# Kernel optimization log

Hardware: AMD Instinct MI355X
Metric: run time of the kernel (lower is better)

## Reference

```python
import jax, jax.numpy as jnp
import numpy as np

EMBED = 1024
HEADS = 16
HEAD_DIM = EMBED // HEADS


def setup_inputs() -> dict:
    key = jax.random.key(0)
    ks = jax.random.split(key, 5)
    s = 1.0 / np.sqrt(EMBED)
    x = jax.random.normal(ks[0], (2, 2048, EMBED), dtype=jnp.float32)
    W_qkv = jax.random.uniform(ks[1], (EMBED, 3 * EMBED), dtype=jnp.float32, minval=-s, maxval=s)
    b_qkv = jax.random.uniform(ks[2], (3 * EMBED,), dtype=jnp.float32, minval=-s, maxval=s)
    W_out = jax.random.uniform(ks[3], (EMBED, EMBED), dtype=jnp.float32, minval=-s, maxval=s)
    b_out = jax.random.uniform(ks[4], (EMBED,), dtype=jnp.float32, minval=-s, maxval=s)
    return {"x": x, "W_qkv": W_qkv, "b_qkv": b_qkv, "W_out": W_out, "b_out": b_out}


def reference(x, W_qkv, b_qkv, W_out, b_out):
    B, S, E = x.shape
    qkv = x @ W_qkv + b_qkv                              # [B,S,3E]
    qkv = qkv.reshape(B, S, 3, HEADS, HEAD_DIM)
    q, k, v = qkv[:, :, 0], qkv[:, :, 1], qkv[:, :, 2]   # [B,S,H,D]
    q = q.transpose(0, 2, 1, 3)                          # [B,H,S,D]
    k = k.transpose(0, 2, 1, 3)
    v = v.transpose(0, 2, 1, 3)
    scale = 1.0 / np.sqrt(HEAD_DIM).astype(np.float32)
    scores = jnp.einsum('bhqd,bhkd->bhqk', q, k) * scale  # [B,H,S,S]
    causal = jnp.tril(jnp.ones((S, S), dtype=bool))
    scores = jnp.where(causal, scores, jnp.float32(-jnp.inf))
    attn = jax.nn.softmax(scores, axis=-1)
    out = jnp.einsum('bhqk,bhkd->bhqd', attn, v)          # [B,H,S,D]
    out = out.transpose(0, 2, 1, 3).reshape(B, S, E)
    return out @ W_out + b_out
```

## Files before the change

kernel.cpp:

```cpp
#include <hip/hip_runtime.h>
#include <hip/hip_bf16.h>
#include <math.h>

typedef __bf16 bf16;
typedef bf16 bf16x4 __attribute__((ext_vector_type(4)));
typedef bf16 bf16x8 __attribute__((ext_vector_type(8)));
typedef float f32x4 __attribute__((ext_vector_type(4)));
typedef float f32x16 __attribute__((ext_vector_type(16)));
typedef unsigned int uint;

#define EMB 1024
#define SEQ 2048
#define BATCH 2
#define NH 16
#define HD 64

#define SCALE2 0.18033688011112042f

__device__ __forceinline__ void glds16(const void* g, void* l) {
  __builtin_amdgcn_global_load_lds(
      (__attribute__((address_space(1))) void*)g,
      (__attribute__((address_space(3))) void*)l, 16, 0, 0);
}

__device__ __forceinline__ uint cvtpk(float lo, float hi) {
  uint r;
  asm("v_cvt_pk_bf16_f32 %0, %1, %2" : "=v"(r) : "v"(lo), "v"(hi));
  return r;
}
__device__ __forceinline__ void plswap(uint& a, uint& b) {
  asm("v_permlane32_swap_b32 %0, %1" : "+v"(a), "+v"(b));
}

__global__ __launch_bounds__(256) void cvt_f32_bf16(const float* __restrict__ in,
                                                    bf16* __restrict__ out, int n) {
  int i = (blockIdx.x * 256 + threadIdx.x) * 4;
  if (i < n) {
    float4 v = *reinterpret_cast<const float4*>(in + i);
    out[i + 0] = (bf16)v.x;
    out[i + 1] = (bf16)v.y;
    out[i + 2] = (bf16)v.z;
    out[i + 3] = (bf16)v.w;
  }
}

__global__ __launch_bounds__(256) void transpose_cvt(const float* __restrict__ in,
                                                     bf16* __restrict__ out,
                                                     int R, int C) {
  __shared__ float tile[32][33];
  int c0 = blockIdx.x * 32, r0 = blockIdx.y * 32;
  int tx = threadIdx.x, ty = threadIdx.y;
#pragma unroll
  for (int i = 0; i < 32; i += 8)
    tile[ty + i][tx] = in[(size_t)(r0 + ty + i) * C + c0 + tx];
  __syncthreads();
#pragma unroll
  for (int i = 0; i < 32; i += 8)
    out[(size_t)(c0 + ty + i) * R + r0 + tx] = (bf16)tile[tx][ty + i];
}

#define QBM 256
#define QBN 128
#define QBK 32

__global__ __launch_bounds__(512) void gemm_qkv(
    const bf16* __restrict__ A, const bf16* __restrict__ Bt,
    const float* __restrict__ bias, int M, int N, int K,
    bf16* __restrict__ outQ, bf16* __restrict__ outK, bf16* __restrict__ outVt) {
  __shared__ bf16 Alds[2][QBM * QBK];
  __shared__ bf16 Blds[2][QBN * QBK];

  const int t = threadIdx.x;
  const int lane = t & 63;
  const int w = t >> 6;
  const int wr = w >> 1, wc = w & 1;
  const int lg = lane >> 4, lr = lane & 15;
  const int m0 = blockIdx.y * QBM;
  const int n0 = blockIdx.x * QBN;

  const int ca0 = t, ca1 = t + 512;
  const int ra0 = ca0 >> 2, cha0 = ca0 & 3;
  const int ra1 = ca1 >> 2, cha1 = ca1 & 3;
  const int rb = t >> 2, chb = t & 3;

  const bf16* Arow0 = A + (size_t)(m0 + ra0) * K + cha0 * 8;
  const bf16* Arow1 = A + (size_t)(m0 + ra1) * K + cha1 * 8;
  const bf16* Brow  = Bt + (size_t)(n0 + rb) * K + chb * 8;

  f32x4 acc[4][4] = {};

  glds16(Arow0, &Alds[0][ca0 * 8]);
  glds16(Arow1, &Alds[0][ca1 * 8]);
  glds16(Brow, &Blds[0][t * 8]);

  int cur = 0;
  for (int k0 = 0; k0 < K; k0 += QBK) {
    if (k0 + QBK < K) {
      const int kn = k0 + QBK;
      const int nb = cur ^ 1;
      glds16(Arow0 + kn, &Alds[nb][ca0 * 8]);
      glds16(Arow1 + kn, &Alds[nb][ca1 * 8]);
      glds16(Brow + kn, &Blds[nb][t * 8]);
      asm volatile("s_waitcnt vmcnt(3)" ::: "memory");
    } else {
      asm volatile("s_waitcnt vmcnt(0)" ::: "memory");
    }
    __builtin_amdgcn_s_barrier();

    bf16x8 af[4], bfr[4];
#pragma unroll
    for (int i = 0; i < 4; ++i)
      af[i] = *reinterpret_cast<const bf16x8*>(
          &Alds[cur][(wr * 64 + i * 16 + lr) * QBK + lg * 8]);
#pragma unroll
    for (int j = 0; j < 4; ++j)
      bfr[j] = *reinterpret_cast<const bf16x8*>(
          &Blds[cur][(wc * 64 + j * 16 + lr) * QBK + lg * 8]);
#pragma unroll
    for (int i = 0; i < 4; ++i)
#pragma unroll
      for (int j = 0; j < 4; ++j)
        acc[i][j] = __builtin_amdgcn_mfma_f32_16x16x32_bf16(af[i], bfr[j], acc[i][j], 0, 0, 0);

    asm volatile("s_waitcnt lgkmcnt(0)" ::: "memory");
    __builtin_amdgcn_s_barrier();
    cur ^= 1;
  }

#pragma unroll
  for (int j = 0; j < 4; ++j) {
    const int n = n0 + wc * 64 + j * 16 + lr;
    const float bi = bias[n];
    const int which = n >> 10, rem = n & 1023;
    const int hh = rem >> 6, d = rem & 63;
#pragma unroll
    for (int i = 0; i < 4; ++i) {
      const int mb = m0 + wr * 64 + i * 16 + lg * 4;
      const int bb = mb >> 11, ss = mb & 2047;
      if (which == 2) {
        bf16x4 pv;
#pragma unroll
        for (int r = 0; r < 4; ++r) pv[r] = (bf16)(acc[i][j][r] + bi);
        *reinterpret_cast<bf16x4*>(
            outVt + (((size_t)bb * NH + hh) * HD + d) * SEQ + ss) = pv;
      } else if (which == 0) {
        bf16* dst = outQ + (((size_t)bb * NH + hh) * SEQ + ss) * HD + d;
#pragma unroll
        for (int r = 0; r < 4; ++r)
          dst[(size_t)r * HD] = (bf16)((acc[i][j][r] + bi) * SCALE2);
      } else {
        bf16* dst = outK + (((size_t)bb * NH + hh) * SEQ + ss) * HD + d;
#pragma unroll
        for (int r = 0; r < 4; ++r) dst[(size_t)r * HD] = (bf16)(acc[i][j][r] + bi);
      }
    }
  }
}

#define BM 128
#define BN 128
#define BK 32

__global__ __launch_bounds__(256) void gemm_proj(
    const bf16* __restrict__ A, const bf16* __restrict__ Bt,
    const float* __restrict__ bias, int M, int N, int K,
    float* __restrict__ outF) {
  __shared__ bf16 Alds[2][BM * BK];
  __shared__ bf16 Blds[2][BM * BK];

  const int t = threadIdx.x;
  const int lane = t & 63;
  const int w = t >> 6;
  const int wr = w >> 1, wc = w & 1;
  const int lg = lane >> 4, lr = lane & 15;
  const int m0 = blockIdx.y * BM;
  const int n0 = blockIdx.x * BN;

  const int c0 = w * 64 + lane;
  const int c1 = 256 + w * 64 + lane;
  const int r0 = c0 >> 2, ch0 = c0 & 3;
  const int r1 = c1 >> 2, ch1 = c1 & 3;

  const bf16* Arow0 = A + (size_t)(m0 + r0) * K + ch0 * 8;
  const bf16* Arow1 = A + (size_t)(m0 + r1) * K + ch1 * 8;
  const bf16* Brow0 = Bt + (size_t)(n0 + r0) * K + ch0 * 8;
  const bf16* Brow1 = Bt + (size_t)(n0 + r1) * K + ch1 * 8;

  f32x4 acc[4][4] = {};

  glds16(Arow0, &Alds[0][c0 * 8]);
  glds16(Arow1, &Alds[0][c1 * 8]);
  glds16(Brow0, &Blds[0][c0 * 8]);
  glds16(Brow1, &Blds[0][c1 * 8]);

  int cur = 0;
  for (int k0 = 0; k0 < K; k0 += BK) {
    if (k0 + BK < K) {
      const int kn = k0 + BK;
      const int nb = cur ^ 1;
      glds16(Arow0 + kn, &Alds[nb][c0 * 8]);
      glds16(Arow1 + kn, &Alds[nb][c1 * 8]);
      glds16(Brow0 + kn, &Blds[nb][c0 * 8]);
      glds16(Brow1 + kn, &Blds[nb][c1 * 8]);
      asm volatile("s_waitcnt vmcnt(4)" ::: "memory");
    } else {
      asm volatile("s_waitcnt vmcnt(0)" ::: "memory");
    }
    __builtin_amdgcn_s_barrier();

    bf16x8 af[4], bfr[4];
#pragma unroll
    for (int i = 0; i < 4; ++i)
      af[i] = *reinterpret_cast<const bf16x8*>(
          &Alds[cur][(wr * 64 + i * 16 + lr) * BK + lg * 8]);
#pragma unroll
    for (int j = 0; j < 4; ++j)
      bfr[j] = *reinterpret_cast<const bf16x8*>(
          &Blds[cur][(wc * 64 + j * 16 + lr) * BK + lg * 8]);
#pragma unroll
    for (int i = 0; i < 4; ++i)
#pragma unroll
      for (int j = 0; j < 4; ++j)
        acc[i][j] = __builtin_amdgcn_mfma_f32_16x16x32_bf16(af[i], bfr[j], acc[i][j], 0, 0, 0);

    asm volatile("s_waitcnt lgkmcnt(0)" ::: "memory");
    __builtin_amdgcn_s_barrier();
    cur ^= 1;
  }

#pragma unroll
  for (int j = 0; j < 4; ++j) {
    const int n = n0 + wc * 64 + j * 16 + lr;
    const float bi = bias[n];
#pragma unroll
    for (int i = 0; i < 4; ++i) {
      const int mb = m0 + wr * 64 + i * 16 + lg * 4;
#pragma unroll
      for (int r = 0; r < 4; ++r)
        outF[(size_t)(mb + r) * N + n] = acc[i][j][r] + bi;
    }
  }
}


#define STAGE(kt_, buf_)                                                       \
  {                                                                            \
    const int kb_ = (kt_) << 7;                                                \
    _Pragma("unroll")                                                          \
    for (int j = 0; j < 4; ++j) {                                              \
      const int g = j * 256 + t;                                               \
      const int rowK = g >> 3, ccK = g & 7;                                    \
      const int pcK = ((ccK ^ (rowK & 7)) << 3);                               \
      glds16(Kb + headoff + (size_t)(kb_ + rowK) * HD + pcK, &Kl[buf_][g * 8]);\
      const int rowV = g >> 4, ccV = g & 15;                                   \
      const int pcV = ((ccV ^ (rowV & 15)) << 3);                              \
      glds16(Vt + headoff + (size_t)rowV * SEQ + kb_ + pcV, &Vl[buf_][g * 8]); \
    }                                                                          \
  }

#define QK_ACC(SX, X)                                                          \
  if (!diag || (X) <= w) {                                                     \
    _Pragma("unroll")                                                          \
    for (int dd = 0; dd < 4; ++dd) {                                           \
      const int pcK = (((dd * 2 + hi) ^ swzK) << 3);                           \
      bf16x8 kf = *reinterpret_cast<const bf16x8*>(                            \
          &Kl[cur][((X) * 32 + l31) * 64 + pcK]);                              \
      SX = __builtin_amdgcn_mfma_f32_32x32x16_bf16(kf, qf[dd], SX, 0, 0, 0);   \
    }                                                                          \
  }

__global__ __launch_bounds__(256, 2) void attn_fwd(
    const bf16* __restrict__ Qb, const bf16* __restrict__ Kb,
    const bf16* __restrict__ Vt, bf16* __restrict__ Ob) {
  __shared__ bf16 Kl[2][128 * 64];
  __shared__ bf16 Vl[2][64 * 128];

  const int t = threadIdx.x;
  const int lane = t & 63;
  const int w = t >> 6;
  const int l31 = lane & 31;
  const int hi = lane >> 5;
  const int hi8 = hi << 3;
  const int swzK = l31 & 7;
  const int swzV = l31 & 15;

  const int id = blockIdx.x;
  const int qb = (id < 256) ? (15 - (id >> 5)) : ((id - 256) >> 5);
  const int bh = id & 31;
  const int h = bh & 15, b = bh >> 4;
  const size_t headoff = ((size_t)b * NH + h) * SEQ * HD;
  const int qrow = qb * 128 + w * 32 + l31;

  bf16x8 qf[4];
  {
    const bf16* qr = Qb + headoff + (size_t)qrow * HD + hi8;
#pragma unroll
    for (int d = 0; d < 4; ++d) qf[d] = *reinterpret_cast<const bf16x8*>(qr + d * 16);
  }

  bf16x8 ones;
#pragma unroll
  for (int i = 0; i < 8; ++i) ones[i] = (bf16)1.0f;

  f32x16 accO0 = {}, accO1 = {};
  f32x16 accL = {};
  const int nkt = qb + 1;

  STAGE(0, 0);

  for (int kt = 0; kt < nkt; ++kt) {
    const int cur = kt & 1;
    if (kt + 1 < nkt) {
      STAGE(kt + 1, cur ^ 1);
      asm volatile("s_waitcnt vmcnt(8)" ::: "memory");
    } else {
      asm volatile("s_waitcnt vmcnt(0)" ::: "memory");
    }
    __builtin_amdgcn_s_barrier();

    const bool diag = (kt == nkt - 1);
    f32x16 s0 = {}, s1 = {}, s2 = {}, s3 = {};
    __builtin_amdgcn_s_setprio(1);
    QK_ACC(s0, 0)
    QK_ACC(s1, 1)
    QK_ACC(s2, 2)
    QK_ACC(s3, 3)
    __builtin_amdgcn_s_setprio(0);
    if (diag) {
      const int kq = (kt << 7) + hi * 4 - qrow;
#pragma unroll
      for (int r = 0; r < 16; ++r) {
        const int off = (r & 3) + 8 * (r >> 2);
        if (kq + off > 0) s0[r] = -1e30f;
        if (kq + off + 32 > 0) s1[r] = -1e30f;
        if (kq + off + 64 > 0) s2[r] = -1e30f;
        if (kq + off + 96 > 0) s3[r] = -1e30f;
      }
    }
#pragma unroll
    for (int r = 0; r < 16; ++r) {
      s0[r] = __builtin_amdgcn_exp2f(s0[r]);
      s1[r] = __builtin_amdgcn_exp2f(s1[r]);
      s2[r] = __builtin_amdgcn_exp2f(s2[r]);
      s3[r] = __builtin_amdgcn_exp2f(s3[r]);
    }
    uint wv[32];
    wv[0]  = cvtpk(s0[0],  s0[1]);  wv[1]  = cvtpk(s0[2],  s0[3]);
    wv[2]  = cvtpk(s0[4],  s0[5]);  wv[3]  = cvtpk(s0[6],  s0[7]);
    wv[4]  = cvtpk(s0[8],  s0[9]);  wv[5]  = cvtpk(s0[10], s0[11]);
    wv[6]  = cvtpk(s0[12], s0[13]); wv[7]  = cvtpk(s0[14], s0[15]);
    wv[8]  = cvtpk(s1[0],  s1[1]);  wv[9]  = cvtpk(s1[2],  s1[3]);
    wv[10] = cvtpk(s1[4],  s1[5]);  wv[11] = cvtpk(s1[6],  s1[7]);
    wv[12] = cvtpk(s1[8],  s1[9]);  wv[13] = cvtpk(s1[10], s1[11]);
    wv[14] = cvtpk(s1[12], s1[13]); wv[15] = cvtpk(s1[14], s1[15]);
    wv[16] = cvtpk(s2[0],  s2[1]);  wv[17] = cvtpk(s2[2],  s2[3]);
    wv[18] = cvtpk(s2[4],  s2[5]);  wv[19] = cvtpk(s2[6],  s2[7]);
    wv[20] = cvtpk(s2[8],  s2[9]);  wv[21] = cvtpk(s2[10], s2[11]);
    wv[22] = cvtpk(s2[12], s2[13]); wv[23] = cvtpk(s2[14], s2[15]);
    wv[24] = cvtpk(s3[0],  s3[1]);  wv[25] = cvtpk(s3[2],  s3[3]);
    wv[26] = cvtpk(s3[4],  s3[5]);  wv[27] = cvtpk(s3[6],  s3[7]);
    wv[28] = cvtpk(s3[8],  s3[9]);  wv[29] = cvtpk(s3[10], s3[11]);
    wv[30] = cvtpk(s3[12], s3[13]); wv[31] = cvtpk(s3[14], s3[15]);
    plswap(wv[0], wv[2]);   plswap(wv[1], wv[3]);
    plswap(wv[4], wv[6]);   plswap(wv[5], wv[7]);
    plswap(wv[8], wv[10]);  plswap(wv[9], wv[11]);
    plswap(wv[12], wv[14]); plswap(wv[13], wv[15]);
    plswap(wv[16], wv[18]); plswap(wv[17], wv[19]);
    plswap(wv[20], wv[22]); plswap(wv[21], wv[23]);
    plswap(wv[24], wv[26]); plswap(wv[25], wv[27]);
    plswap(wv[28], wv[30]); plswap(wv[29], wv[31]);
    __builtin_amdgcn_s_setprio(1);
#pragma unroll
    for (int ks = 0; ks < 8; ++ks) {
      if (!diag || ks < 2 * w + 2) {
        uint4 u = make_uint4(wv[(ks >> 1) * 8 + (ks & 1) * 4],
                             wv[(ks >> 1) * 8 + (ks & 1) * 4 + 1],
                             wv[(ks >> 1) * 8 + (ks & 1) * 4 + 2],
                             wv[(ks >> 1) * 8 + (ks & 1) * 4 + 3]);
        bf16x8 pf = *reinterpret_cast<bf16x8*>(&u);
        const int pcV = (((ks * 2 + hi) ^ swzV) << 3);
        bf16x8 vf0 = *reinterpret_cast<const bf16x8*>(&Vl[cur][l31 * 128 + pcV]);
        bf16x8 vf1 = *reinterpret_cast<const bf16x8*>(&Vl[cur][(l31 + 32) * 128 + pcV]);
        accO0 = __builtin_amdgcn_mfma_f32_32x32x16_bf16(vf0, pf, accO0, 0, 0, 0);
        accO1 = __builtin_amdgcn_mfma_f32_32x32x16_bf16(vf1, pf, accO1, 0, 0, 0);
        accL  = __builtin_amdgcn_mfma_f32_32x32x16_bf16(ones, pf, accL, 0, 0, 0);
      }
    }
    __builtin_amdgcn_s_setprio(0);
    asm volatile("s_waitcnt lgkmcnt(0)" ::: "memory");
    __builtin_amdgcn_s_barrier();
  }

  const float inv = 1.0f / accL[0];
  bf16* orow = Ob + ((size_t)b * SEQ + qrow) * EMB + h * HD + hi * 4;
#pragma unroll
  for (int rq = 0; rq < 4; ++rq) {
    bf16x4 o0, o1;
#pragma unroll
    for (int i = 0; i < 4; ++i) {
      o0[i] = (bf16)(accO0[rq * 4 + i] * inv);
      o1[i] = (bf16)(accO1[rq * 4 + i] * inv);
    }
    *reinterpret_cast<bf16x4*>(orow + rq * 8) = o0;
    *reinterpret_cast<bf16x4*>(orow + 32 + rq * 8) = o1;
  }
}

extern "C" void kernel_launch(void* const* d_in, const int* in_sizes, int n_in,
                              void* d_out, int out_size, void* d_ws, size_t ws_size,
                              hipStream_t stream) {
  const float* x    = (const float*)d_in[0];
  const float* Wqkv = (const float*)d_in[1];
  const float* bqkv = (const float*)d_in[2];
  const float* Wout = (const float*)d_in[3];
  const float* bout = (const float*)d_in[4];
  float* out = (float*)d_out;

  char* ws = (char*)d_ws;
  bf16* xb     = (bf16*)(ws);
  bf16* wqkvt  = (bf16*)(ws + 8388608);
  bf16* woutt  = (bf16*)(ws + 14680064);
  bf16* Qb     = (bf16*)(ws + 16777216);
  bf16* Kb     = (bf16*)(ws + 25165824);
  bf16* Vtb    = (bf16*)(ws + 33554432);
  bf16* attnb  = (bf16*)(ws + 41943040);

  const int n1 = 4096 * 1024;
  cvt_f32_bf16<<<(n1 / 4 + 255) / 256, 256, 0, stream>>>(x, xb, n1);
  dim3 tb(32, 8);
  transpose_cvt<<<dim3(3072 / 32, 1024 / 32), tb, 0, stream>>>(Wqkv, wqkvt, 1024, 3072);
  transpose_cvt<<<dim3(1024 / 32, 1024 / 32), tb, 0, stream>>>(Wout, woutt, 1024, 1024);

  dim3 g1(3072 / QBN, 4096 / QBM);
  gemm_qkv<<<g1, 512, 0, stream>>>(xb, wqkvt, bqkv, 4096, 3072, 1024,
                                   Qb, Kb, Vtb);

  attn_fwd<<<512, 256, 0, stream>>>(Qb, Kb, Vtb, attnb);

  dim3 g2(1024 / BN, 4096 / BM);
  gemm_proj<<<g2, 256, 0, stream>>>(attnb, woutt, bout, 4096, 1024, 1024, out);
}
```

Measured before the change: 116.4 us.

## Split causal attention KV range across two blocks and add combine kernel

The attention kernel now splits each query block's key range into two halves handled by separate workgroups, doubling the grid. It shrinks the key tile from 128 to 64 and raises the occupancy hint to four blocks per CU. Each half writes unnormalized bf16 partial outputs and per-row sums. A new elementwise kernel adds the two partials and divides by the summed denominators. This aims to improve load balance and CU utilisation for the causal triangle. In exchange it adds an extra launch, extra global traffic for the partials, and a bf16 rounding of unnormalized values.

```diff
diff --git a/kernel.cpp b/kernel.cpp
--- a/kernel.cpp
+++ b/kernel.cpp
@@ -242,38 +242,27 @@
   }
 }
 
-
-#define STAGE(kt_, buf_)                                                       \
+#define AKT 64
+
+#define ASTAGE(kt_, buf_)                                                      \
   {                                                                            \
-    const int kb_ = (kt_) << 7;                                                \
+    const int kb_ = (kt_) << 6;                                                \
     _Pragma("unroll")                                                          \
-    for (int j = 0; j < 4; ++j) {                                              \
+    for (int j = 0; j < 2; ++j) {                                              \
       const int g = j * 256 + t;                                               \
-      const int rowK = g >> 3, ccK = g & 7;                                    \
-      const int pcK = ((ccK ^ (rowK & 7)) << 3);                               \
-      glds16(Kb + headoff + (size_t)(kb_ + rowK) * HD + pcK, &Kl[buf_][g * 8]);\
-      const int rowV = g >> 4, ccV = g & 15;                                   \
-      const int pcV = ((ccV ^ (rowV & 15)) << 3);                              \
-      glds16(Vt + headoff + (size_t)rowV * SEQ + kb_ + pcV, &Vl[buf_][g * 8]); \
+      const int row = g >> 3, cc = g & 7;                                      \
+      const int pc = ((cc ^ (row & 7)) << 3);                                  \
+      glds16(Kb + headoff + (size_t)(kb_ + row) * HD + pc, &Kl[buf_][g * 8]);  \
+      glds16(Vt + headoff + (size_t)row * SEQ + kb_ + pc, &Vl[buf_][g * 8]);   \
     }                                                                          \
   }
 
-#define QK_ACC(SX, X)                                                          \
-  if (!diag || (X) <= w) {                                                     \
-    _Pragma("unroll")                                                          \
-    for (int dd = 0; dd < 4; ++dd) {                                           \
-      const int pcK = (((dd * 2 + hi) ^ swzK) << 3);                           \
-      bf16x8 kf = *reinterpret_cast<const bf16x8*>(                            \
-          &Kl[cur][((X) * 32 + l31) * 64 + pcK]);                              \
-      SX = __builtin_amdgcn_mfma_f32_32x32x16_bf16(kf, qf[dd], SX, 0, 0, 0);   \
-    }                                                                          \
-  }
-
-__global__ __launch_bounds__(256, 2) void attn_fwd(
+__global__ __launch_bounds__(256, 4) void attn_fwd(
     const bf16* __restrict__ Qb, const bf16* __restrict__ Kb,
-    const bf16* __restrict__ Vt, bf16* __restrict__ Ob) {
-  __shared__ bf16 Kl[2][128 * 64];
-  __shared__ bf16 Vl[2][64 * 128];
+    const bf16* __restrict__ Vt, bf16* __restrict__ P0,
+    bf16* __restrict__ P1, float* __restrict__ Lbuf) {
+  __shared__ bf16 Kl[2][64 * 64];
+  __shared__ bf16 Vl[2][64 * 64];
 
   const int t = threadIdx.x;
   const int lane = t & 63;
@@ -281,15 +270,16 @@
   const int l31 = lane & 31;
   const int hi = lane >> 5;
   const int hi8 = hi << 3;
-  const int swzK = l31 & 7;
-  const int swzV = l31 & 15;
+  const int swz = l31 & 7;
 
   const int id = blockIdx.x;
-  const int qb = (id < 256) ? (15 - (id >> 5)) : ((id - 256) >> 5);
-  const int bh = id & 31;
-  const int h = bh & 15, b = bh >> 4;
+  const int qhb = id >> 1, split = id & 1;
+  const int qb = 15 - (qhb >> 5);
+  const int hb = qhb & 31;
+  const int h = hb & 15, b = hb >> 4;
   const size_t headoff = ((size_t)b * NH + h) * SEQ * HD;
-  const int qrow = qb * 128 + w * 32 + l31;
+  const int qw0 = qb * 128 + w * 32;
+  const int qrow = qw0 + l31;
 
   bf16x8 qf[4];
   {
@@ -304,106 +294,122 @@
 
   f32x16 accO0 = {}, accO1 = {};
   f32x16 accL = {};
-  const int nkt = qb + 1;
-
-  STAGE(0, 0);
-
-  for (int kt = 0; kt < nkt; ++kt) {
-    const int cur = kt & 1;
-    if (kt + 1 < nkt) {
-      STAGE(kt + 1, cur ^ 1);
-      asm volatile("s_waitcnt vmcnt(8)" ::: "memory");
+  const int kt0 = split ? (qb + 1) : 0;
+  const int kt1 = split ? (2 * qb + 2) : (qb + 1);
+
+  ASTAGE(kt0, 0);
+
+  int i = 0;
+  for (int kt = kt0; kt < kt1; ++kt, ++i) {
+    const int cur = i & 1;
+    if (kt + 1 < kt1) {
+      ASTAGE(kt + 1, cur ^ 1);
+      asm volatile("s_waitcnt vmcnt(4)" ::: "memory");
     } else {
       asm volatile("s_waitcnt vmcnt(0)" ::: "memory");
     }
     __builtin_amdgcn_s_barrier();
 
-    const bool diag = (kt == nkt - 1);
-    f32x16 s0 = {}, s1 = {}, s2 = {}, s3 = {};
-    __builtin_amdgcn_s_setprio(1);
-    QK_ACC(s0, 0)
-    QK_ACC(s1, 1)
-    QK_ACC(s2, 2)
-    QK_ACC(s3, 3)
-    __builtin_amdgcn_s_setprio(0);
-    if (diag) {
-      const int kq = (kt << 7) + hi * 4 - qrow;
+    const int k0 = kt << 6;
+    if (k0 <= qw0 + 31) {
+      f32x16 s0 = {}, s1 = {};
+      __builtin_amdgcn_s_setprio(1);
+#pragma unroll
+      for (int dd = 0; dd < 4; ++dd) {
+        const int pc = (((dd * 2 + hi) ^ swz) << 3);
+        bf16x8 kf0 = *reinterpret_cast<const bf16x8*>(&Kl[cur][l31 * 64 + pc]);
+        s0 = __builtin_amdgcn_mfma_f32_32x32x16_bf16(kf0, qf[dd], s0, 0, 0, 0);
+      }
+      if (k0 + 32 <= qw0 + 31) {
+#pragma unroll
+        for (int dd = 0; dd < 4; ++dd) {
+          const int pc = (((dd * 2 + hi) ^ swz) << 3);
+          bf16x8 kf1 = *reinterpret_cast<const bf16x8*>(&Kl[cur][(l31 + 32) * 64 + pc]);
+          s1 = __builtin_amdgcn_mfma_f32_32x32x16_bf16(kf1, qf[dd], s1, 0, 0, 0);
+        }
+      }
+      __builtin_amdgcn_s_setprio(0);
+      if (k0 + 63 > qw0) {
+        const int kq = k0 + hi * 4 - qrow;
+#pragma unroll
+        for (int r = 0; r < 16; ++r) {
+          const int off = (r & 3) + 8 * (r >> 2);
+          if (kq + off > 0) s0[r] = -1e30f;
+          if (kq + off + 32 > 0) s1[r] = -1e30f;
+        }
+      }
 #pragma unroll
       for (int r = 0; r < 16; ++r) {
-        const int off = (r & 3) + 8 * (r >> 2);
-        if (kq + off > 0) s0[r] = -1e30f;
-        if (kq + off + 32 > 0) s1[r] = -1e30f;
-        if (kq + off + 64 > 0) s2[r] = -1e30f;
-        if (kq + off + 96 > 0) s3[r] = -1e30f;
-      }
-    }
-#pragma unroll
-    for (int r = 0; r < 16; ++r) {
-      s0[r] = __builtin_amdgcn_exp2f(s0[r]);
-      s1[r] = __builtin_amdgcn_exp2f(s1[r]);
-      s2[r] = __builtin_amdgcn_exp2f(s2[r]);
-      s3[r] = __builtin_amdgcn_exp2f(s3[r]);
-    }
-    uint wv[32];
-    wv[0]  = cvtpk(s0[0],  s0[1]);  wv[1]  = cvtpk(s0[2],  s0[3]);
-    wv[2]  = cvtpk(s0[4],  s0[5]);  wv[3]  = cvtpk(s0[6],  s0[7]);
-    wv[4]  = cvtpk(s0[8],  s0[9]);  wv[5]  = cvtpk(s0[10], s0[11]);
-    wv[6]  = cvtpk(s0[12], s0[13]); wv[7]  = cvtpk(s0[14], s0[15]);
-    wv[8]  = cvtpk(s1[0],  s1[1]);  wv[9]  = cvtpk(s1[2],  s1[3]);
-    wv[10] = cvtpk(s1[4],  s1[5]);  wv[11] = cvtpk(s1[6],  s1[7]);
-    wv[12] = cvtpk(s1[8],  s1[9]);  wv[13] = cvtpk(s1[10], s1[11]);
-    wv[14] = cvtpk(s1[12], s1[13]); wv[15] = cvtpk(s1[14], s1[15]);
-    wv[16] = cvtpk(s2[0],  s2[1]);  wv[17] = cvtpk(s2[2],  s2[3]);
-    wv[18] = cvtpk(s2[4],  s2[5]);  wv[19] = cvtpk(s2[6],  s2[7]);
-    wv[20] = cvtpk(s2[8],  s2[9]);  wv[21] = cvtpk(s2[10], s2[11]);
-    wv[22] = cvtpk(s2[12], s2[13]); wv[23] = cvtpk(s2[14], s2[15]);
-    wv[24] = cvtpk(s3[0],  s3[1]);  wv[25] = cvtpk(s3[2],  s3[3]);
-    wv[26] = cvtpk(s3[4],  s3[5]);  wv[27] = cvtpk(s3[6],  s3[7]);
-    wv[28] = cvtpk(s3[8],  s3[9]);  wv[29] = cvtpk(s3[10], s3[11]);
-    wv[30] = cvtpk(s3[12], s3[13]); wv[31] = cvtpk(s3[14], s3[15]);
-    plswap(wv[0], wv[2]);   plswap(wv[1], wv[3]);
-    plswap(wv[4], wv[6]);   plswap(wv[5], wv[7]);
-    plswap(wv[8], wv[10]);  plswap(wv[9], wv[11]);
-    plswap(wv[12], wv[14]); plswap(wv[13], wv[15]);
-    plswap(wv[16], wv[18]); plswap(wv[17], wv[19]);
-    plswap(wv[20], wv[22]); plswap(wv[21], wv[23]);
-    plswap(wv[24], wv[26]); plswap(wv[25], wv[27]);
-    plswap(wv[28], wv[30]); plswap(wv[29], wv[31]);
-    __builtin_amdgcn_s_setprio(1);
-#pragma unroll
-    for (int ks = 0; ks < 8; ++ks) {
-      if (!diag || ks < 2 * w + 2) {
-        uint4 u = make_uint4(wv[(ks >> 1) * 8 + (ks & 1) * 4],
-                             wv[(ks >> 1) * 8 + (ks & 1) * 4 + 1],
-                             wv[(ks >> 1) * 8 + (ks & 1) * 4 + 2],
-                             wv[(ks >> 1) * 8 + (ks & 1) * 4 + 3]);
-        bf16x8 pf = *reinterpret_cast<bf16x8*>(&u);
-        const int pcV = (((ks * 2 + hi) ^ swzV) << 3);
-        bf16x8 vf0 = *reinterpret_cast<const bf16x8*>(&Vl[cur][l31 * 128 + pcV]);
-        bf16x8 vf1 = *reinterpret_cast<const bf16x8*>(&Vl[cur][(l31 + 32) * 128 + pcV]);
-        accO0 = __builtin_amdgcn_mfma_f32_32x32x16_bf16(vf0, pf, accO0, 0, 0, 0);
-        accO1 = __builtin_amdgcn_mfma_f32_32x32x16_bf16(vf1, pf, accO1, 0, 0, 0);
-        accL  = __builtin_amdgcn_mfma_f32_32x32x16_bf16(ones, pf, accL, 0, 0, 0);
-      }
-    }
-    __builtin_amdgcn_s_setprio(0);
+        s0[r] = __builtin_amdgcn_exp2f(s0[r]);
+        s1[r] = __builtin_amdgcn_exp2f(s1[r]);
+      }
+      uint wv[16];
+      wv[0]  = cvtpk(s0[0],  s0[1]);  wv[1]  = cvtpk(s0[2],  s0[3]);
+      wv[2]  = cvtpk(s0[4],  s0[5]);  wv[3]  = cvtpk(s0[6],  s0[7]);
+      wv[4]  = cvtpk(s0[8],  s0[9]);  wv[5]  = cvtpk(s0[10], s0[11]);
+      wv[6]  = cvtpk(s0[12], s0[13]); wv[7]  = cvtpk(s0[14], s0[15]);
+      wv[8]  = cvtpk(s1[0],  s1[1]);  wv[9]  = cvtpk(s1[2],  s1[3]);
+      wv[10] = cvtpk(s1[4],  s1[5]);  wv[11] = cvtpk(s1[6],  s1[7]);
+      wv[12] = cvtpk(s1[8],  s1[9]);  wv[13] = cvtpk(s1[10], s1[11]);
+      wv[14] = cvtpk(s1[12], s1[13]); wv[15] = cvtpk(s1[14], s1[15]);
+      plswap(wv[0], wv[2]);   plswap(wv[1], wv[3]);
+      plswap(wv[4], wv[6]);   plswap(wv[5], wv[7]);
+      plswap(wv[8], wv[10]);  plswap(wv[9], wv[11]);
+      plswap(wv[12], wv[14]); plswap(wv[13], wv[15]);
+      __builtin_amdgcn_s_setprio(1);
+#pragma unroll
+      for (int ks = 0; ks < 4; ++ks) {
+        if (k0 + ks * 16 <= qw0 + 31) {
+          uint4 u = make_uint4(wv[ks * 4], wv[ks * 4 + 1], wv[ks * 4 + 2], wv[ks * 4 + 3]);
+          bf16x8 pf = *reinterpret_cast<bf16x8*>(&u);
+          const int pc = (((ks * 2 + hi) ^ swz) << 3);
+          bf16x8 vf0 = *reinterpret_cast<const bf16x8*>(&Vl[cur][l31 * 64 + pc]);
+          bf16x8 vf1 = *reinterpret_cast<const bf16x8*>(&Vl[cur][(l31 + 32) * 64 + pc]);
+          accO0 = __builtin_amdgcn_mfma_f32_32x32x16_bf16(vf0, pf, accO0, 0, 0, 0);
+          accO1 = __builtin_amdgcn_mfma_f32_32x32x16_bf16(vf1, pf, accO1, 0, 0, 0);
+          accL  = __builtin_amdgcn_mfma_f32_32x32x16_bf16(ones, pf, accL, 0, 0, 0);
+        }
+      }
+      __builtin_amdgcn_s_setprio(0);
+    }
     asm volatile("s_waitcnt lgkmcnt(0)" ::: "memory");
     __builtin_amdgcn_s_barrier();
   }
 
-  const float inv = 1.0f / accL[0];
-  bf16* orow = Ob + ((size_t)b * SEQ + qrow) * EMB + h * HD + hi * 4;
+  bf16* Pout = split ? P1 : P0;
+  bf16* orow = Pout + ((size_t)b * SEQ + qrow) * EMB + h * HD + hi * 4;
 #pragma unroll
   for (int rq = 0; rq < 4; ++rq) {
     bf16x4 o0, o1;
 #pragma unroll
-    for (int i = 0; i < 4; ++i) {
-      o0[i] = (bf16)(accO0[rq * 4 + i] * inv);
-      o1[i] = (bf16)(accO1[rq * 4 + i] * inv);
+    for (int i2 = 0; i2 < 4; ++i2) {
+      o0[i2] = (bf16)accO0[rq * 4 + i2];
+      o1[i2] = (bf16)accO1[rq * 4 + i2];
     }
     *reinterpret_cast<bf16x4*>(orow + rq * 8) = o0;
     *reinterpret_cast<bf16x4*>(orow + 32 + rq * 8) = o1;
   }
+  if (hi == 0)
+    Lbuf[(((size_t)split * BATCH + b) * NH + h) * SEQ + qrow] = accL[0];
+}
+
+__global__ __launch_bounds__(256) void attn_combine(
+    const bf16* __restrict__ P0, const bf16* __restrict__ P1,
+    const float* __restrict__ Lbuf, bf16* __restrict__ Ob) {
+  const int idx = (blockIdx.x * 256 + threadIdx.x) * 8;
+  const int row = idx >> 10;
+  const int col = idx & 1023;
+  const int h = col >> 6;
+  const int b = row >> 11, s = row & 2047;
+  const size_t lidx = (((size_t)b * NH + h) * SEQ + s);
+  const float l = Lbuf[lidx] + Lbuf[(size_t)BATCH * NH * SEQ + lidx];
+  const float inv = 1.0f / l;
+  bf16x8 a = *reinterpret_cast<const bf16x8*>(P0 + idx);
+  bf16x8 c = *reinterpret_cast<const bf16x8*>(P1 + idx);
+  bf16x8 o;
+#pragma unroll
+  for (int j = 0; j < 8; ++j) o[j] = (bf16)(((float)a[j] + (float)c[j]) * inv);
+  *reinterpret_cast<bf16x8*>(Ob + idx) = o;
 }
 
 extern "C" void kernel_launch(void* const* d_in, const int* in_sizes, int n_in,
@@ -424,6 +430,8 @@
   bf16* Kb     = (bf16*)(ws + 25165824);
   bf16* Vtb    = (bf16*)(ws + 33554432);
   bf16* attnb  = (bf16*)(ws + 41943040);
+  bf16* P0     = xb;
+  float* Lbuf  = (float*)(ws + 8388608);
 
   const int n1 = 4096 * 1024;
   cvt_f32_bf16<<<(n1 / 4 + 255) / 256, 256, 0, stream>>>(x, xb, n1);
@@ -435,7 +443,8 @@
   gemm_qkv<<<g1, 512, 0, stream>>>(xb, wqkvt, bqkv, 4096, 3072, 1024,
                                    Qb, Kb, Vtb);
 
-  attn_fwd<<<512, 256, 0, stream>>>(Qb, Kb, Vtb, attnb);
+  attn_fwd<<<1024, 256, 0, stream>>>(Qb, Kb, Vtb, P0, attnb, Lbuf);
+  attn_combine<<<2048, 256, 0, stream>>>(P0, attnb, Lbuf, attnb);
 
   dim3 g2(1024 / BN, 4096 / BM);
   gemm_proj<<<g2, 256, 0, stream>>>(attnb, woutt, bout, 4096, 1024, 1024, out);
```

After: 118.7 us. Within noise of the previous version (+2.0%).

## Enlarge QKV GEMM tile to 256x256x64 with swizzled LDS and phased MFMA schedule

Applied to the files above, without the earlier changes.

The QKV projection GEMM tile grows from 256x128x32 to 256x256x64, and each of the 8 waves now owns a 128x64 output slice. LDS loads use an XOR swizzle to avoid bank conflicts. Each k-step is split into four phases that interleave next-tile global-to-LDS staging with MFMA bursts under raised wave priority (s_setprio). The goal is better operand reuse and overlap of loads with compute, at the cost of more registers, more LDS (64KB per block), extra barriers and fewer blocks in the grid.

```diff
diff --git a/kernel.cpp b/kernel.cpp
--- a/kernel.cpp
+++ b/kernel.cpp
@@ -60,8 +60,53 @@
 }
 
 #define QBM 256
-#define QBN 128
-#define QBK 32
+#define QBN 256
+#define QBK 64
+
+#define QSTG(PTR, LDSBUF, KT_)                                                 \
+  _Pragma("unroll")                                                            \
+  for (int c = 0; c < 4; ++c) {                                                \
+    const int g = c * 512 + t;                                                 \
+    const int row = g >> 3, ch = g & 7;                                        \
+    const int pc = (ch ^ (row & 7)) << 3;                                      \
+    glds16(PTR + (size_t)row * K + (KT_) * QBK + pc, &LDSBUF[g * 8]);          \
+  }
+
+#define QPHASE(MH, NH, STG)                                                    \
+  {                                                                            \
+    bf16x8 af[4][2], bfr[2][2];                                                \
+    _Pragma("unroll")                                                          \
+    for (int i = 0; i < 4; ++i) {                                              \
+      const int row = wr * 128 + ((MH) * 4 + i) * 16 + lr;                     \
+      _Pragma("unroll")                                                        \
+      for (int kk = 0; kk < 2; ++kk)                                           \
+        af[i][kk] = *reinterpret_cast<const bf16x8*>(                          \
+            &Alds[cur][row * 64 + (((kk * 4 + lg) ^ (row & 7)) << 3)]);        \
+    }                                                                          \
+    _Pragma("unroll")                                                          \
+    for (int jn = 0; jn < 2; ++jn) {                                           \
+      const int rowb = wc * 64 + ((NH) * 2 + jn) * 16 + lr;                    \
+      _Pragma("unroll")                                                        \
+      for (int kk = 0; kk < 2; ++kk)                                           \
+        bfr[jn][kk] = *reinterpret_cast<const bf16x8*>(                        \
+            &Blds[cur][rowb * 64 + (((kk * 4 + lg) ^ (rowb & 7)) << 3)]);      \
+    }                                                                          \
+    STG;                                                                       \
+    __builtin_amdgcn_s_barrier();                                              \
+    __builtin_amdgcn_s_setprio(1);                                             \
+    _Pragma("unroll")                                                          \
+    for (int i = 0; i < 4; ++i)                                                \
+      _Pragma("unroll")                                                        \
+      for (int jn = 0; jn < 2; ++jn)                                           \
+        _Pragma("unroll")                                                      \
+        for (int kk = 0; kk < 2; ++kk)                                         \
+          acc[(MH) * 4 + i][(NH) * 2 + jn] =                                   \
+              __builtin_amdgcn_mfma_f32_16x16x32_bf16(                         \
+                  af[i][kk], bfr[jn][kk], acc[(MH) * 4 + i][(NH) * 2 + jn],    \
+                  0, 0, 0);                                                    \
+    __builtin_amdgcn_s_setprio(0);                                             \
+    __builtin_amdgcn_s_barrier();                                              \
+  }
 
 __global__ __launch_bounds__(512) void gemm_qkv(
     const bf16* __restrict__ A, const bf16* __restrict__ Bt,
@@ -73,85 +118,57 @@
   const int t = threadIdx.x;
   const int lane = t & 63;
   const int w = t >> 6;
-  const int wr = w >> 1, wc = w & 1;
+  const int wr = w >> 2, wc = w & 3;
   const int lg = lane >> 4, lr = lane & 15;
   const int m0 = blockIdx.y * QBM;
   const int n0 = blockIdx.x * QBN;
 
-  const int ca0 = t, ca1 = t + 512;
-  const int ra0 = ca0 >> 2, cha0 = ca0 & 3;
-  const int ra1 = ca1 >> 2, cha1 = ca1 & 3;
-  const int rb = t >> 2, chb = t & 3;
-
-  const bf16* Arow0 = A + (size_t)(m0 + ra0) * K + cha0 * 8;
-  const bf16* Arow1 = A + (size_t)(m0 + ra1) * K + cha1 * 8;
-  const bf16* Brow  = Bt + (size_t)(n0 + rb) * K + chb * 8;
-
-  f32x4 acc[4][4] = {};
-
-  glds16(Arow0, &Alds[0][ca0 * 8]);
-  glds16(Arow1, &Alds[0][ca1 * 8]);
-  glds16(Brow, &Blds[0][t * 8]);
+  const bf16* Aptr = A + (size_t)m0 * K;
+  const bf16* Bptr = Bt + (size_t)n0 * K;
+
+  f32x4 acc[8][4] = {};
+  const int NT = K / QBK;
+
+  QSTG(Aptr, (&Alds[0][0]), 0);
+  QSTG(Bptr, (&Blds[0][0]), 0);
 
   int cur = 0;
-  for (int k0 = 0; k0 < K; k0 += QBK) {
-    if (k0 + QBK < K) {
-      const int kn = k0 + QBK;
-      const int nb = cur ^ 1;
-      glds16(Arow0 + kn, &Alds[nb][ca0 * 8]);
-      glds16(Arow1 + kn, &Alds[nb][ca1 * 8]);
-      glds16(Brow + kn, &Blds[nb][t * 8]);
-      asm volatile("s_waitcnt vmcnt(3)" ::: "memory");
-    } else {
-      asm volatile("s_waitcnt vmcnt(0)" ::: "memory");
-    }
+  for (int kt = 0; kt < NT; ++kt) {
+    asm volatile("s_waitcnt vmcnt(0)" ::: "memory");
     __builtin_amdgcn_s_barrier();
-
-    bf16x8 af[4], bfr[4];
-#pragma unroll
-    for (int i = 0; i < 4; ++i)
-      af[i] = *reinterpret_cast<const bf16x8*>(
-          &Alds[cur][(wr * 64 + i * 16 + lr) * QBK + lg * 8]);
-#pragma unroll
-    for (int j = 0; j < 4; ++j)
-      bfr[j] = *reinterpret_cast<const bf16x8*>(
-          &Blds[cur][(wc * 64 + j * 16 + lr) * QBK + lg * 8]);
-#pragma unroll
-    for (int i = 0; i < 4; ++i)
-#pragma unroll
-      for (int j = 0; j < 4; ++j)
-        acc[i][j] = __builtin_amdgcn_mfma_f32_16x16x32_bf16(af[i], bfr[j], acc[i][j], 0, 0, 0);
-
-    asm volatile("s_waitcnt lgkmcnt(0)" ::: "memory");
-    __builtin_amdgcn_s_barrier();
+    const bool more = (kt + 1 < NT);
+    QPHASE(0, 0, if (more) { QSTG(Aptr, (&Alds[cur ^ 1][0]), kt + 1); })
+    QPHASE(0, 1, if (more) { QSTG(Bptr, (&Blds[cur ^ 1][0]), kt + 1); })
+    QPHASE(1, 0, )
+    QPHASE(1, 1, )
     cur ^= 1;
   }
 
 #pragma unroll
-  for (int j = 0; j < 4; ++j) {
-    const int n = n0 + wc * 64 + j * 16 + lr;
+  for (int jn = 0; jn < 4; ++jn) {
+    const int n = n0 + wc * 64 + jn * 16 + lr;
     const float bi = bias[n];
     const int which = n >> 10, rem = n & 1023;
     const int hh = rem >> 6, d = rem & 63;
 #pragma unroll
-    for (int i = 0; i < 4; ++i) {
-      const int mb = m0 + wr * 64 + i * 16 + lg * 4;
+    for (int i = 0; i < 8; ++i) {
+      const int mb = m0 + wr * 128 + i * 16 + lg * 4;
       const int bb = mb >> 11, ss = mb & 2047;
       if (which == 2) {
         bf16x4 pv;
 #pragma unroll
-        for (int r = 0; r < 4; ++r) pv[r] = (bf16)(acc[i][j][r] + bi);
+        for (int r = 0; r < 4; ++r) pv[r] = (bf16)(acc[i][jn][r] + bi);
         *reinterpret_cast<bf16x4*>(
             outVt + (((size_t)bb * NH + hh) * HD + d) * SEQ + ss) = pv;
       } else if (which == 0) {
         bf16* dst = outQ + (((size_t)bb * NH + hh) * SEQ + ss) * HD + d;
 #pragma unroll
         for (int r = 0; r < 4; ++r)
-          dst[(size_t)r * HD] = (bf16)((acc[i][j][r] + bi) * SCALE2);
+          dst[(size_t)r * HD] = (bf16)((acc[i][jn][r] + bi) * SCALE2);
       } else {
         bf16* dst = outK + (((size_t)bb * NH + hh) * SEQ + ss) * HD + d;
 #pragma unroll
-        for (int r = 0; r < 4; ++r) dst[(size_t)r * HD] = (bf16)(acc[i][j][r] + bi);
+        for (int r = 0; r < 4; ++r) dst[(size_t)r * HD] = (bf16)(acc[i][jn][r] + bi);
       }
     }
   }
@@ -241,7 +258,6 @@
     }
   }
 }
-
 
 #define STAGE(kt_, buf_)                                                       \
   {                                                                            \
```

Measured after the change: 121.9 us. +4.7%, slower.
